# Performance work log

Hardware: AMD Instinct MI355X
Metric: run time of the kernel (lower is better)

## Reference

```python
import jax, jax.numpy as jnp
import numpy as np

# (in_dim, out_dim) for fc1..fc14, hard-coded in the torch module
DIMS = [(12,12),(12,11),(11,10),(10,9),(9,8),(8,7),(7,6),(6,7),(7,8),(8,9),(9,10),(10,11),(11,12),(12,2)]
BATCH = 2_000_000


def setup_inputs() -> dict:
    key = jax.random.key(0)
    keys = jax.random.split(key, 2 * len(DIMS) + 1)
    inp = {"x": jax.random.normal(keys[0], (BATCH, 12), dtype=jnp.float32)}
    for i, (din, dout) in enumerate(DIMS):
        s = 1.0 / np.sqrt(din)  # torch nn.Linear default init range
        inp[f"w{i+1}"] = jax.random.uniform(keys[2*i+1], (dout, din), jnp.float32, -s, s)
        inp[f"b{i+1}"] = jax.random.uniform(keys[2*i+2], (dout,), jnp.float32, -s, s)
    return inp


def _forward(x, Ws, Bs):
    lin = lambda h, i: h @ Ws[i].T + Bs[i]
    # encoder half: fc1..fc6 with ReLU, saving identities 1..6
    ids = []
    h = x
    for i in range(6):
        h = jax.nn.relu(lin(h, i))
        ids.append(h)
    # bottleneck fc7
    h = jax.nn.relu(lin(h, 6))
    # decoder half: fc8..fc13, each adds the matching identity before ReLU
    # fc8 (+id6), fc9 (+id5), ..., fc13 (+id1)
    for i in range(7, 13):
        h = jax.nn.relu(lin(h, i) + ids[12 - i])
    # fc14 + softmax over class dim
    return jax.nn.softmax(lin(h, 13), axis=1)


def reference(x, w1, b1, w2, b2, w3, b3, w4, b4, w5, b5, w6, b6, w7, b7,
              w8, b8, w9, b9, w10, b10, w11, b11, w12, b12, w13, b13, w14, b14):
    Ws = [w1, w2, w3, w4, w5, w6, w7, w8, w9, w10, w11, w12, w13, w14]
    Bs = [b1, b2, b3, b4, b5, b6, b7, b8, b9, b10, b11, b12, b13, b14]
    return _forward(x, Ws, Bs)
```

## Files before the change

### kernel.cpp

```cpp
#include <hip/hip_runtime.h>
#include <math.h>

#define DEV __device__ __forceinline__

template <int DIN, int DOUT>
DEV void lin(const float* __restrict__ w, const float* __restrict__ b,
             const float* in, float* out) {
#pragma unroll
    for (int o = 0; o < DOUT; ++o) {
        float acc = b[o];
#pragma unroll
        for (int k = 0; k < DIN; ++k) {
            acc = fmaf(in[k], w[o * DIN + k], acc);
        }
        out[o] = acc;
    }
}

template <int N>
DEV void relu_ip(float* v) {
#pragma unroll
    for (int k = 0; k < N; ++k) v[k] = fmaxf(v[k], 0.0f);
}

template <int N>
DEV void add_relu_ip(float* v, const float* s) {
#pragma unroll
    for (int k = 0; k < N; ++k) v[k] = fmaxf(v[k] + s[k], 0.0f);
}

__global__ void __launch_bounds__(256)
csnet14_kernel(const float* __restrict__ x,
               const float* __restrict__ w1,  const float* __restrict__ b1,
               const float* __restrict__ w2,  const float* __restrict__ b2,
               const float* __restrict__ w3,  const float* __restrict__ b3,
               const float* __restrict__ w4,  const float* __restrict__ b4,
               const float* __restrict__ w5,  const float* __restrict__ b5,
               const float* __restrict__ w6,  const float* __restrict__ b6,
               const float* __restrict__ w7,  const float* __restrict__ b7,
               const float* __restrict__ w8,  const float* __restrict__ b8,
               const float* __restrict__ w9,  const float* __restrict__ b9,
               const float* __restrict__ w10, const float* __restrict__ b10,
               const float* __restrict__ w11, const float* __restrict__ b11,
               const float* __restrict__ w12, const float* __restrict__ b12,
               const float* __restrict__ w13, const float* __restrict__ b13,
               const float* __restrict__ w14, const float* __restrict__ b14,
               float* __restrict__ out, int n) {
    int i = blockIdx.x * blockDim.x + threadIdx.x;
    if (i >= n) return;

    const float4* xr = reinterpret_cast<const float4*>(x + (size_t)i * 12);
    float4 v0 = xr[0];
    float4 v1 = xr[1];
    float4 v2 = xr[2];
    float h0[12] = {v0.x, v0.y, v0.z, v0.w,
                    v1.x, v1.y, v1.z, v1.w,
                    v2.x, v2.y, v2.z, v2.w};

    float id1[12]; lin<12, 12>(w1, b1, h0,  id1); relu_ip<12>(id1);
    float id2[11]; lin<12, 11>(w2, b2, id1, id2); relu_ip<11>(id2);
    float id3[10]; lin<11, 10>(w3, b3, id2, id3); relu_ip<10>(id3);
    float id4[9];  lin<10,  9>(w4, b4, id3, id4); relu_ip<9>(id4);
    float id5[8];  lin< 9,  8>(w5, b5, id4, id5); relu_ip<8>(id5);
    float id6[7];  lin< 8,  7>(w6, b6, id5, id6); relu_ip<7>(id6);

    float t7[6];   lin< 7,  6>(w7, b7, id6, t7);  relu_ip<6>(t7);

    float t8[7];   lin< 6,  7>(w8,  b8,  t7,  t8);  add_relu_ip<7>(t8,  id6);
    float t9[8];   lin< 7,  8>(w9,  b9,  t8,  t9);  add_relu_ip<8>(t9,  id5);
    float t10[9];  lin< 8,  9>(w10, b10, t9,  t10); add_relu_ip<9>(t10, id4);
    float t11[10]; lin< 9, 10>(w11, b11, t10, t11); add_relu_ip<10>(t11, id3);
    float t12[11]; lin<10, 11>(w12, b12, t11, t12); add_relu_ip<11>(t12, id2);
    float t13[12]; lin<11, 12>(w13, b13, t12, t13); add_relu_ip<12>(t13, id1);

    float l[2];    lin<12,  2>(w14, b14, t13, l);
    float m  = fmaxf(l[0], l[1]);
    float e0 = __expf(l[0] - m);
    float e1 = __expf(l[1] - m);
    float inv = __builtin_amdgcn_rcpf(e0 + e1);

    float2 o;
    o.x = e0 * inv;
    o.y = e1 * inv;
    reinterpret_cast<float2*>(out)[i] = o;
}

extern "C" void kernel_launch(void* const* d_in, const int* in_sizes, int n_in,
                              void* d_out, int out_size, void* d_ws, size_t ws_size,
                              hipStream_t stream) {
    const float* x   = (const float*)d_in[0];
    const float* w1  = (const float*)d_in[1];  const float* b1  = (const float*)d_in[2];
    const float* w2  = (const float*)d_in[3];  const float* b2  = (const float*)d_in[4];
    const float* w3  = (const float*)d_in[5];  const float* b3  = (const float*)d_in[6];
    const float* w4  = (const float*)d_in[7];  const float* b4  = (const float*)d_in[8];
    const float* w5  = (const float*)d_in[9];  const float* b5  = (const float*)d_in[10];
    const float* w6  = (const float*)d_in[11]; const float* b6  = (const float*)d_in[12];
    const float* w7  = (const float*)d_in[13]; const float* b7  = (const float*)d_in[14];
    const float* w8  = (const float*)d_in[15]; const float* b8  = (const float*)d_in[16];
    const float* w9  = (const float*)d_in[17]; const float* b9  = (const float*)d_in[18];
    const float* w10 = (const float*)d_in[19]; const float* b10 = (const float*)d_in[20];
    const float* w11 = (const float*)d_in[21]; const float* b11 = (const float*)d_in[22];
    const float* w12 = (const float*)d_in[23]; const float* b12 = (const float*)d_in[24];
    const float* w13 = (const float*)d_in[25]; const float* b13 = (const float*)d_in[26];
    const float* w14 = (const float*)d_in[27]; const float* b14 = (const float*)d_in[28];
    float* out = (float*)d_out;

    const int n = in_sizes[0] / 12;
    dim3 block(256);
    dim3 grid((n + 255) / 256);
    csnet14_kernel<<<grid, block, 0, stream>>>(
        x, w1, b1, w2, b2, w3, b3, w4, b4, w5, b5, w6, b6, w7, b7,
        w8, b8, w9, b9, w10, b10, w11, b11, w12, b12, w13, b13, w14, b14,
        out, n);
}
```

Measured before the change: 252.2 us.

## Rewrite MLP forward as fp16 MFMA chain with prepacked weight tiles

Replaces the per-thread scalar FMA chain with a persistent wave kernel that runs each layer as a 32x32x16 fp16 MFMA. Weights and biases are packed once by a small prep kernel into padded fp16 A-fragments, with the bias folded in through a constant-one input column. Activations are repacked between layers with cross-lane permutes. The aim is to cut the large VALU FMA count, at the cost of fp16 precision in weights and activations and a hard-coded tile count tied to the batch size.

```diff
diff --git a/kernel.cpp b/kernel.cpp
--- a/kernel.cpp
+++ b/kernel.cpp
@@ -3,113 +3,170 @@
 
 #define DEV __device__ __forceinline__
 
-template <int DIN, int DOUT>
-DEV void lin(const float* __restrict__ w, const float* __restrict__ b,
-             const float* in, float* out) {
-#pragma unroll
-    for (int o = 0; o < DOUT; ++o) {
-        float acc = b[o];
-#pragma unroll
-        for (int k = 0; k < DIN; ++k) {
-            acc = fmaf(in[k], w[o * DIN + k], acc);
-        }
-        out[o] = acc;
-    }
+
+typedef _Float16 f16x8 __attribute__((ext_vector_type(8)));
+typedef _Float16 h2 __attribute__((ext_vector_type(2)));
+typedef float f32x16 __attribute__((ext_vector_type(16)));
+
+union BU { f16x8 v; h2 p[4]; };
+
+DEV h2 pk2(float a, float b) {
+    auto t = __builtin_amdgcn_cvt_pkrtz(a, b);
+    h2 r;
+    __builtin_memcpy(&r, &t, 4);
+    return r;
 }
 
-template <int N>
-DEV void relu_ip(float* v) {
-#pragma unroll
-    for (int k = 0; k < N; ++k) v[k] = fmaxf(v[k], 0.0f);
+DEV h2 bperm(int addr, h2 v) {
+    int x;
+    __builtin_memcpy(&x, &v, 4);
+    int y = __builtin_amdgcn_ds_bpermute(addr, x);
+    h2 r;
+    __builtin_memcpy(&r, &y, 4);
+    return r;
 }
 
-template <int N>
-DEV void add_relu_ip(float* v, const float* s) {
-#pragma unroll
-    for (int k = 0; k < N; ++k) v[k] = fmaxf(v[k] + s[k], 0.0f);
+DEV f16x8 mk_b(const float* h, bool hi, int xaddr) {
+    h2 P01 = pk2(h[0], h[1]);
+    h2 P23 = pk2(h[2], h[3]);
+    h2 P45 = pk2(h[4], h[5]);
+    h2 P67 = pk2(h[6], h[7]);
+    h2 sA = hi ? P01 : P45;
+    h2 sB = hi ? P23 : P67;
+    h2 pA = bperm(xaddr, sA);
+    h2 pB = bperm(xaddr, sB);
+    const h2 ONES = {(_Float16)1.0f, (_Float16)0.0f};
+    const h2 ZER  = {(_Float16)0.0f, (_Float16)0.0f};
+    BU u;
+    u.p[0] = hi ? pA : P01;
+    u.p[1] = hi ? pB : P23;
+    u.p[2] = hi ? ONES : pA;
+    u.p[3] = hi ? ZER : pB;
+    return u.v;
 }
 
+struct SrcPtrs { const float* p[28]; };
+
 __global__ void __launch_bounds__(256)
-csnet14_kernel(const float* __restrict__ x,
-               const float* __restrict__ w1,  const float* __restrict__ b1,
-               const float* __restrict__ w2,  const float* __restrict__ b2,
-               const float* __restrict__ w3,  const float* __restrict__ b3,
-               const float* __restrict__ w4,  const float* __restrict__ b4,
-               const float* __restrict__ w5,  const float* __restrict__ b5,
-               const float* __restrict__ w6,  const float* __restrict__ b6,
-               const float* __restrict__ w7,  const float* __restrict__ b7,
-               const float* __restrict__ w8,  const float* __restrict__ b8,
-               const float* __restrict__ w9,  const float* __restrict__ b9,
-               const float* __restrict__ w10, const float* __restrict__ b10,
-               const float* __restrict__ w11, const float* __restrict__ b11,
-               const float* __restrict__ w12, const float* __restrict__ b12,
-               const float* __restrict__ w13, const float* __restrict__ b13,
-               const float* __restrict__ w14, const float* __restrict__ b14,
-               float* __restrict__ out, int n) {
-    int i = blockIdx.x * blockDim.x + threadIdx.x;
-    if (i >= n) return;
+build_a(SrcPtrs ps, f16x8* __restrict__ ws) {
+    int t = blockIdx.x * blockDim.x + threadIdx.x;
+    if (t >= 14 * 64) return;
+    int L = t >> 6, lane = t & 63, m = lane & 31, hi = lane >> 5;
+    const int DIN[14]  = {12, 12, 11, 10, 9, 8, 7, 6, 7, 8, 9, 10, 11, 12};
+    const int DOUT[14] = {12, 11, 10, 9, 8, 7, 6, 7, 8, 9, 10, 11, 12, 2};
+    const float* w = ps.p[2 * L];
+    const float* b = ps.p[2 * L + 1];
+    f16x8 f;
+#pragma unroll
+    for (int j = 0; j < 8; ++j) {
+        int k = hi * 8 + j;
+        float v = 0.0f;
+        if (m < DOUT[L]) {
+            if (k < DIN[L]) v = w[m * DIN[L] + k];
+            else if (k == 12) v = b[m];
+        }
+        f[j] = (_Float16)v;
+    }
+    ws[t] = f;
+}
 
-    const float4* xr = reinterpret_cast<const float4*>(x + (size_t)i * 12);
-    float4 v0 = xr[0];
-    float4 v1 = xr[1];
-    float4 v2 = xr[2];
-    float h0[12] = {v0.x, v0.y, v0.z, v0.w,
-                    v1.x, v1.y, v1.z, v1.w,
-                    v2.x, v2.y, v2.z, v2.w};
+#define NTILES 62500
 
-    float id1[12]; lin<12, 12>(w1, b1, h0,  id1); relu_ip<12>(id1);
-    float id2[11]; lin<12, 11>(w2, b2, id1, id2); relu_ip<11>(id2);
-    float id3[10]; lin<11, 10>(w3, b3, id2, id3); relu_ip<10>(id3);
-    float id4[9];  lin<10,  9>(w4, b4, id3, id4); relu_ip<9>(id4);
-    float id5[8];  lin< 9,  8>(w5, b5, id4, id5); relu_ip<8>(id5);
-    float id6[7];  lin< 8,  7>(w6, b6, id5, id6); relu_ip<7>(id6);
+__global__ void __launch_bounds__(256)
+csnet14_mfma(const float* __restrict__ x, const f16x8* __restrict__ ws,
+             float* __restrict__ out, int nwaves) {
+    const int tid  = blockIdx.x * blockDim.x + threadIdx.x;
+    const int wave = tid >> 6;
+    const int lane = threadIdx.x & 63;
+    const int n    = lane & 31;
+    const bool hi  = (lane >> 5) != 0;
+    const int xadr = (lane ^ 32) * 4;
 
-    float t7[6];   lin< 7,  6>(w7, b7, id6, t7);  relu_ip<6>(t7);
+    f16x8 A[14];
+#pragma unroll
+    for (int L = 0; L < 14; ++L) A[L] = ws[L * 64 + lane];
 
-    float t8[7];   lin< 6,  7>(w8,  b8,  t7,  t8);  add_relu_ip<7>(t8,  id6);
-    float t9[8];   lin< 7,  8>(w9,  b9,  t8,  t9);  add_relu_ip<8>(t9,  id5);
-    float t10[9];  lin< 8,  9>(w10, b10, t9,  t10); add_relu_ip<9>(t10, id4);
-    float t11[10]; lin< 9, 10>(w11, b11, t10, t11); add_relu_ip<10>(t11, id3);
-    float t12[11]; lin<10, 11>(w12, b12, t11, t12); add_relu_ip<11>(t12, id2);
-    float t13[12]; lin<11, 12>(w13, b13, t12, t13); add_relu_ip<12>(t13, id1);
+    const f32x16 zacc = {};
 
-    float l[2];    lin<12,  2>(w14, b14, t13, l);
-    float m  = fmaxf(l[0], l[1]);
-    float e0 = __expf(l[0] - m);
-    float e1 = __expf(l[1] - m);
-    float inv = __builtin_amdgcn_rcpf(e0 + e1);
+    for (int tile = wave; tile < NTILES; tile += nwaves) {
+        const int b0 = tile * 32;
 
-    float2 o;
-    o.x = e0 * inv;
-    o.y = e1 * inv;
-    reinterpret_cast<float2*>(out)[i] = o;
+        const float4* xb = reinterpret_cast<const float4*>(x + (size_t)(b0 + n) * 12);
+        float4 a  = xb[hi ? 2 : 0];
+        float4 bq = xb[1];
+        const h2 ONES = {(_Float16)1.0f, (_Float16)0.0f};
+        const h2 ZER  = {(_Float16)0.0f, (_Float16)0.0f};
+        BU u;
+        u.p[0] = pk2(a.x, a.y);
+        u.p[1] = pk2(a.z, a.w);
+        u.p[2] = hi ? ONES : pk2(bq.x, bq.y);
+        u.p[3] = hi ? ZER  : pk2(bq.z, bq.w);
+        f16x8 B = u.v;
+
+        f32x16 C;
+        float id1[8], id2[8], id3[8], id4[8], id5[8], id6[8], h[8];
+
+#define ENC(L, IDARR)                                                        \
+        C = __builtin_amdgcn_mfma_f32_32x32x16_f16(A[L], B, zacc, 0, 0, 0);  \
+        _Pragma("unroll")                                                    \
+        for (int r = 0; r < 8; ++r) IDARR[r] = fmaxf(C[r], 0.0f);            \
+        B = mk_b(IDARR, hi, xadr);
+
+        ENC(0, id1)
+        ENC(1, id2)
+        ENC(2, id3)
+        ENC(3, id4)
+        ENC(4, id5)
+        ENC(5, id6)
+
+        C = __builtin_amdgcn_mfma_f32_32x32x16_f16(A[6], B, zacc, 0, 0, 0);
+#pragma unroll
+        for (int r = 0; r < 8; ++r) h[r] = fmaxf(C[r], 0.0f);
+        B = mk_b(h, hi, xadr);
+
+#define DEC(L, IDARR)                                                        \
+        C = __builtin_amdgcn_mfma_f32_32x32x16_f16(A[L], B, zacc, 0, 0, 0);  \
+        _Pragma("unroll")                                                    \
+        for (int r = 0; r < 8; ++r) h[r] = fmaxf(C[r] + IDARR[r], 0.0f);     \
+        B = mk_b(h, hi, xadr);
+
+        DEC(7,  id6)
+        DEC(8,  id5)
+        DEC(9,  id4)
+        DEC(10, id3)
+        DEC(11, id2)
+        DEC(12, id1)
+
+        C = __builtin_amdgcn_mfma_f32_32x32x16_f16(A[13], B, zacc, 0, 0, 0);
+        if (!hi) {
+            float l0 = C[0], l1 = C[1];
+            float mx = fmaxf(l0, l1);
+            float e0 = __expf(l0 - mx);
+            float e1 = __expf(l1 - mx);
+            float inv = __builtin_amdgcn_rcpf(e0 + e1);
+            float2 o;
+            o.x = e0 * inv;
+            o.y = e1 * inv;
+            reinterpret_cast<float2*>(out)[b0 + n] = o;
+        }
+    }
+#undef ENC
+#undef DEC
 }
 
 extern "C" void kernel_launch(void* const* d_in, const int* in_sizes, int n_in,
                               void* d_out, int out_size, void* d_ws, size_t ws_size,
                               hipStream_t stream) {
-    const float* x   = (const float*)d_in[0];
-    const float* w1  = (const float*)d_in[1];  const float* b1  = (const float*)d_in[2];
-    const float* w2  = (const float*)d_in[3];  const float* b2  = (const float*)d_in[4];
-    const float* w3  = (const float*)d_in[5];  const float* b3  = (const float*)d_in[6];
-    const float* w4  = (const float*)d_in[7];  const float* b4  = (const float*)d_in[8];
-    const float* w5  = (const float*)d_in[9];  const float* b5  = (const float*)d_in[10];
-    const float* w6  = (const float*)d_in[11]; const float* b6  = (const float*)d_in[12];
-    const float* w7  = (const float*)d_in[13]; const float* b7  = (const float*)d_in[14];
-    const float* w8  = (const float*)d_in[15]; const float* b8  = (const float*)d_in[16];
-    const float* w9  = (const float*)d_in[17]; const float* b9  = (const float*)d_in[18];
-    const float* w10 = (const float*)d_in[19]; const float* b10 = (const float*)d_in[20];
-    const float* w11 = (const float*)d_in[21]; const float* b11 = (const float*)d_in[22];
-    const float* w12 = (const float*)d_in[23]; const float* b12 = (const float*)d_in[24];
-    const float* w13 = (const float*)d_in[25]; const float* b13 = (const float*)d_in[26];
-    const float* w14 = (const float*)d_in[27]; const float* b14 = (const float*)d_in[28];
+    const float* x = (const float*)d_in[0];
     float* out = (float*)d_out;
+    f16x8* ws = (f16x8*)d_ws;
 
-    const int n = in_sizes[0] / 12;
-    dim3 block(256);
-    dim3 grid((n + 255) / 256);
-    csnet14_kernel<<<grid, block, 0, stream>>>(
-        x, w1, b1, w2, b2, w3, b3, w4, b4, w5, b5, w6, b6, w7, b7,
-        w8, b8, w9, b9, w10, b10, w11, b11, w12, b12, w13, b13, w14, b14,
-        out, n);
+    SrcPtrs ps;
+    for (int i = 0; i < 28; ++i) ps.p[i] = (const float*)d_in[1 + i];
+
+    build_a<<<4, 256, 0, stream>>>(ps, ws);
+
+    const int nblocks = 1024;
+    const int nwaves  = nblocks * (256 / 64);
+    csnet14_mfma<<<nblocks, 256, 0, stream>>>(x, ws, out, nwaves);
 }
```

After: 249.1 us. Within noise of the previous version (-1.2%).
